# Performance work log

Measured on AMD Instinct MI355X. Metric: run time of the kernel, lower is better.

Reference implementation:

```python
import jax, jax.numpy as jnp
import numpy as np

D_MODEL = 1024
N_HEADS = 16
D_HIDDEN = 4096
EPS = 1e-6
SCALE = float(np.sqrt(D_MODEL // N_HEADS))


def setup_inputs() -> dict:
    key = jax.random.key(0)
    ks = jax.random.split(key, 12)
    d, h = D_MODEL, D_HIDDEN
    init = lambda k, shape, fan_in: jax.random.uniform(k, shape, jnp.float32, -1.0, 1.0) / np.sqrt(fan_in)
    return {
        "x": jax.random.normal(ks[0], (2, 2048, d), jnp.float32),
        "W_q": init(ks[1], (d, d), d),
        "W_k": init(ks[2], (d, d), d),
        "W_v": init(ks[3], (d, d), d),
        "W_o": init(ks[4], (d, d), d),
        "b_o": init(ks[5], (d,), d),
        "attn_norm_w": 1.0 + jax.random.normal(ks[6], (d,), jnp.float32) / np.sqrt(d),
        "ffn_norm_w": 1.0 + jax.random.normal(ks[7], (d,), jnp.float32) / np.sqrt(d),
        "W_gate": init(ks[8], (d, h), d),
        "W_hidden": init(ks[9], (d, h), d),
        "W_out": init(ks[10], (h, d), h),
        "b_out": init(ks[11], (d,), h),
    }


def rmsnorm(x, w):
    return w * x * jax.lax.rsqrt(jnp.mean(x * x, axis=-1, keepdims=True) + EPS)


def attention(x, W_q, W_k, W_v, W_o, b_o):
    b, l, d = x.shape
    hd = d // N_HEADS
    split = lambda t: t.reshape(b, l, N_HEADS, hd).transpose(0, 2, 1, 3)  # b n l d
    q = split(x @ W_q)
    k = split(x @ W_k)
    v = split(x @ W_v)
    scores = jnp.einsum('bnld,bnmd->bnlm', q, k) / SCALE
    attn = jax.nn.softmax(scores, axis=-1)
    out = jnp.einsum('bnlm,bnmd->bnld', attn, v)
    out = out.transpose(0, 2, 1, 3).reshape(b, l, d)
    return out @ W_o + b_o


def swiglu(x, W_gate, W_hidden, W_out, b_out):
    return (jax.nn.silu(x @ W_gate) * (x @ W_hidden)) @ W_out + b_out


def reference(x, W_q, W_k, W_v, W_o, b_o, attn_norm_w, ffn_norm_w, W_gate, W_hidden, W_out, b_out):
    x = x + attention(rmsnorm(x, attn_norm_w), W_q, W_k, W_v, W_o, b_o)
    return x + swiglu(rmsnorm(x, ffn_norm_w), W_gate, W_hidden, W_out, b_out)
```

## Files before the change

kernel.cpp:

```cpp
#include <hip/hip_runtime.h>
#include <stdint.h>
#include <stddef.h>

typedef unsigned short ushort_t;
typedef __attribute__((ext_vector_type(8))) unsigned short us8;
typedef __attribute__((ext_vector_type(4))) unsigned short us4;
typedef __attribute__((ext_vector_type(2))) unsigned int u32x2;
typedef __attribute__((ext_vector_type(8))) short bf16x8;
typedef __attribute__((ext_vector_type(4))) float f32x4;
typedef __attribute__((ext_vector_type(4))) float f4;

#define DM 1024
#define SEQ 2048
#define NBATCH 2
#define NHEADS 16
#define HDIM 64
#define DH 4096
#define ROWS 4096

__device__ __forceinline__ float bf2f(ushort_t u) {
  union { unsigned int i; float f; } v; v.i = ((unsigned int)u) << 16; return v.f;
}
__device__ __forceinline__ ushort_t f2bf(float f) {
  union { float f; unsigned int i; } v; v.f = f;
  unsigned int x = v.i;
  unsigned int r = (x + 0x7FFFu + ((x >> 16) & 1u)) >> 16;
  return (ushort_t)r;
}
__device__ __forceinline__ unsigned int fbits(float f) {
  union { float f; unsigned int i; } v; v.f = f; return v.i;
}

__global__ void transpose_all(const float* __restrict__ Wq, const float* __restrict__ Wk,
                              const float* __restrict__ Wv, const float* __restrict__ Wo,
                              const float* __restrict__ Wg, const float* __restrict__ Wh,
                              const float* __restrict__ Wu,
                              ushort_t* __restrict__ WqkvT, ushort_t* __restrict__ WoT,
                              ushort_t* __restrict__ WghT, ushort_t* __restrict__ WuT) {
  const float* src; ushort_t* dst; int R, C, rowmul = 1, rowoff = 0;
  switch (blockIdx.y) {
    case 0: src = Wq; dst = WqkvT;                R = DM; C = DM; break;
    case 1: src = Wk; dst = WqkvT + DM * DM;      R = DM; C = DM; break;
    case 2: src = Wv; dst = WqkvT + 2 * DM * DM;  R = DM; C = DM; break;
    case 3: src = Wo; dst = WoT;                  R = DM; C = DM; break;
    case 4: src = Wg; dst = WghT;                 R = DM; C = DH; rowmul = 2; rowoff = 0; break;
    case 5: src = Wh; dst = WghT;                 R = DM; C = DH; rowmul = 2; rowoff = 1; break;
    default: src = Wu; dst = WuT;                 R = DH; C = DM; break;
  }
  int nbx = C >> 6, nby = R >> 6;
  int bid = blockIdx.x;
  if (bid >= nbx * nby) return;
  int c0 = (bid % nbx) * 64, r0 = (bid / nbx) * 64;

  __shared__ ushort_t tile[64][68];
  int t = threadIdx.x;
#pragma unroll
  for (int i = 0; i < 4; ++i) {
    int c = i * 256 + t;
    int row = c >> 4, col4 = (c & 15) * 4;
    f4 v = *(const f4*)(src + (size_t)(r0 + row) * C + c0 + col4);
#pragma unroll
    for (int j = 0; j < 4; ++j) tile[row][col4 + j] = f2bf(v[j]);
  }
  __syncthreads();
#pragma unroll
  for (int i = 0; i < 4; ++i) {
    int c = i * 256 + t;
    int orow = c >> 4, col4 = (c & 15) * 4;
    us4 v;
#pragma unroll
    for (int j = 0; j < 4; ++j) v[j] = tile[col4 + j][orow];
    *(us4*)(dst + ((size_t)(c0 + orow) * rowmul + rowoff) * R + r0 + col4) = v;
  }
}

__global__ void rmsnorm_kernel(const float* __restrict__ x,
                               const float* __restrict__ w,
                               ushort_t* __restrict__ y) {
  int row = blockIdx.x;
  int t = threadIdx.x;
  f4 xv = *(const f4*)(x + (size_t)row * DM + t * 4);
  float s = 0.f;
#pragma unroll
  for (int j = 0; j < 4; ++j) s += xv[j] * xv[j];
#pragma unroll
  for (int off = 32; off >= 1; off >>= 1) s += __shfl_xor(s, off);
  __shared__ float wsum[4];
  if ((t & 63) == 0) wsum[t >> 6] = s;
  __syncthreads();
  float tot = wsum[0] + wsum[1] + wsum[2] + wsum[3];
  float scale = rsqrtf(tot * (1.0f / DM) + 1e-6f);
  f4 wv = *(const f4*)(w + t * 4);
  us4 o;
#pragma unroll
  for (int j = 0; j < 4; ++j) o[j] = f2bf(xv[j] * wv[j] * scale);
  *(us4*)(y + (size_t)row * DM + t * 4) = o;
}

template <int EPI, int TM>
__global__ __launch_bounds__(256) void gemm_bt(
    const ushort_t* __restrict__ A, const ushort_t* __restrict__ Bt,
    void* __restrict__ Cv, int M, int N, int K,
    const float* __restrict__ bias, const void* __restrict__ resv) {
  constexpr int FI = TM / 32;
  __shared__ __align__(16) ushort_t As[TM * 64];
  __shared__ __align__(16) ushort_t Bs[128 * 64];
  int tid = threadIdx.x;
  int l = tid & 63, w = tid >> 6;
  int wm = w >> 1, wn = w & 1;
  int m0 = blockIdx.y * TM, n0 = blockIdx.x * 128;
  int lr = l & 15, lk = (l >> 4) * 8;
  f32x4 acc[FI][4] = {};
  const ushort_t* Ag = A + (size_t)m0 * K;
  const ushort_t* Bg = Bt + (size_t)n0 * K;
  int srow = tid >> 3;
  int scol = (tid & 7) * 8;

  for (int kt = 0; kt < K; kt += 64) {
#pragma unroll
    for (int i = 0; i < TM / 32; ++i) {
      __builtin_amdgcn_global_load_lds(
          (const __attribute__((address_space(1))) unsigned int*)(Ag + (size_t)(i * 32 + srow) * K + kt + scol),
          (__attribute__((address_space(3))) unsigned int*)(&As[(i * 256 + tid) * 8]), 16, 0, 0);
    }
#pragma unroll
    for (int i = 0; i < 4; ++i) {
      __builtin_amdgcn_global_load_lds(
          (const __attribute__((address_space(1))) unsigned int*)(Bg + (size_t)(i * 32 + srow) * K + kt + scol),
          (__attribute__((address_space(3))) unsigned int*)(&Bs[(i * 256 + tid) * 8]), 16, 0, 0);
    }
    __syncthreads();
#pragma unroll
    for (int kk = 0; kk < 2; ++kk) {
      bf16x8 a[FI], b[4];
#pragma unroll
      for (int i = 0; i < FI; ++i)
        a[i] = *(const bf16x8*)(&As[(wm * (TM / 2) + i * 16 + lr) * 64 + kk * 32 + lk]);
#pragma unroll
      for (int j = 0; j < 4; ++j)
        b[j] = *(const bf16x8*)(&Bs[(wn * 64 + j * 16 + lr) * 64 + kk * 32 + lk]);
#pragma unroll
      for (int i = 0; i < FI; ++i)
#pragma unroll
        for (int j = 0; j < 4; ++j)
          acc[i][j] = __builtin_amdgcn_mfma_f32_16x16x32_bf16(a[i], b[j], acc[i][j], 0, 0, 0);
    }
    __syncthreads();
  }

  int r0 = (l >> 4) * 4;
#pragma unroll
  for (int i = 0; i < FI; ++i) {
#pragma unroll
    for (int r = 0; r < 4; ++r) {
      int grow = m0 + wm * (TM / 2) + i * 16 + r0 + r;
#pragma unroll
      for (int j = 0; j < 4; ++j) {
        int gcol = n0 + wn * 64 + j * 16 + lr;
        float v = acc[i][j][r];
        if (EPI == 0) {
          ((ushort_t*)Cv)[(size_t)grow * N + gcol] = f2bf(v);
        } else if (EPI == 1) {
          size_t idx = (size_t)grow * N + gcol;
          float r2 = ((const float*)resv)[idx];
          ((float*)Cv)[idx] = v + bias[gcol] + r2;
        } else {
          float o = __shfl_xor(v, 1);
          float gt = (lr & 1) ? o : v;
          float hd = (lr & 1) ? v : o;
          float a = gt / (1.0f + __expf(-gt)) * hd;
          if (!(lr & 1))
            ((ushort_t*)Cv)[(size_t)grow * (N >> 1) + (gcol >> 1)] = f2bf(a);
        }
      }
    }
  }
}

__global__ void vtrans_kernel(const ushort_t* __restrict__ qkv,
                              ushort_t* __restrict__ VT) {
  __shared__ ushort_t tile[64][72];
  int t = threadIdx.x;
  int s0 = blockIdx.x * 64;
  int h = blockIdx.y, b = blockIdx.z;
  const ushort_t* src = qkv + (size_t)b * SEQ * (3 * DM) + 2 * DM + h * HDIM;
  ushort_t* dst = VT + ((size_t)(b * NHEADS + h) * HDIM) * SEQ;
#pragma unroll
  for (int i = 0; i < 2; ++i) {
    int c = i * 256 + t;
    int srow = c >> 3, d8 = (c & 7) * 8;
    *(us8*)(&tile[srow][d8]) = *(const us8*)(src + (size_t)(s0 + srow) * (3 * DM) + d8);
  }
  __syncthreads();
#pragma unroll
  for (int i = 0; i < 2; ++i) {
    int c = i * 256 + t;
    int drow = c >> 3, s8 = (c & 7) * 8;
    us8 v;
#pragma unroll
    for (int j = 0; j < 8; ++j) v[j] = tile[s8 + j][drow];
    *(us8*)(dst + (size_t)drow * SEQ + s0 + s8) = v;
  }
}

#define LDP 72

__global__ __launch_bounds__(256) void attn_mfma(
    const ushort_t* __restrict__ Qp, const ushort_t* __restrict__ Kp,
    const ushort_t* __restrict__ VT, ushort_t* __restrict__ Op,
    int qs, int os) {
  __shared__ __align__(16) ushort_t Qs[64 * LDP];
  __shared__ __align__(16) ushort_t Ks[64 * LDP];
  __shared__ __align__(16) ushort_t Vs[64 * LDP];
  __shared__ __align__(16) ushort_t Ps[4][16 * LDP];
  int tid = threadIdx.x;
  int l = tid & 63;
  int w = tid >> 6;
  int g = l >> 4;
  int q = l & 15;
  int h = blockIdx.y, b = blockIdx.z;
  int q0 = blockIdx.x * 64;
  const size_t base = (size_t)b * SEQ * qs + h * HDIM;
  const size_t obase = (size_t)b * SEQ * os + h * HDIM;
  const ushort_t* Vb = VT + ((size_t)(b * NHEADS + h) * HDIM) * SEQ;

#pragma unroll
  for (int i = 0; i < 2; ++i) {
    int cc = i * 256 + tid;
    int row = cc >> 3, d8 = (cc & 7) * 8;
    *(us8*)(&Qs[row * LDP + d8]) =
        *(const us8*)(Qp + base + (size_t)(q0 + row) * qs + d8);
  }
  __syncthreads();
  bf16x8 qf0 = *(const bf16x8*)(&Qs[(w * 16 + q) * LDP + g * 8]);
  bf16x8 qf1 = *(const bf16x8*)(&Qs[(w * 16 + q) * LDP + 32 + g * 8]);

  const float C1 = 0.125f * 1.44269504f;
  const float C2 = 12.0f * 1.44269504f;
  float l_run = 0.f;
  f32x4 oacc[4] = {};

  for (int kv = 0; kv < SEQ; kv += 64) {
    __syncthreads();
#pragma unroll
    for (int i = 0; i < 2; ++i) {
      int cc = i * 256 + tid;
      int row = cc >> 3, d8 = (cc & 7) * 8;
      *(us8*)(&Ks[row * LDP + d8]) =
          *(const us8*)(Kp + base + (size_t)(kv + row) * qs + d8);
      *(us8*)(&Vs[row * LDP + d8]) =
          *(const us8*)(Vb + (size_t)row * SEQ + kv + d8);
    }
    __syncthreads();

    f32x4 sacc[4] = {};
#pragma unroll
    for (int t = 0; t < 4; ++t) {
      bf16x8 kf0 = *(const bf16x8*)(&Ks[(t * 16 + q) * LDP + g * 8]);
      sacc[t] = __builtin_amdgcn_mfma_f32_16x16x32_bf16(kf0, qf0, sacc[t], 0, 0, 0);
      bf16x8 kf1 = *(const bf16x8*)(&Ks[(t * 16 + q) * LDP + 32 + g * 8]);
      sacc[t] = __builtin_amdgcn_mfma_f32_16x16x32_bf16(kf1, qf1, sacc[t], 0, 0, 0);
    }

    float psum = 0.f;
#pragma unroll
    for (int t = 0; t < 4; ++t) {
      float p0 = exp2f(fmaf(sacc[t][0], C1, -C2));
      float p1 = exp2f(fmaf(sacc[t][1], C1, -C2));
      float p2 = exp2f(fmaf(sacc[t][2], C1, -C2));
      float p3 = exp2f(fmaf(sacc[t][3], C1, -C2));
      psum += (p0 + p1) + (p2 + p3);
      u32x2 d;
      d[0] = __builtin_amdgcn_perm(fbits(p1), fbits(p0), 0x07060302u);
      d[1] = __builtin_amdgcn_perm(fbits(p3), fbits(p2), 0x07060302u);
      *(u32x2*)(&Ps[w][q * LDP + t * 16 + g * 4]) = d;
    }
    l_run += psum;

    __asm__ volatile("s_waitcnt lgkmcnt(0)" ::: "memory");

#pragma unroll
    for (int kk = 0; kk < 2; ++kk) {
      bf16x8 pf = *(const bf16x8*)(&Ps[w][q * LDP + kk * 32 + g * 8]);
#pragma unroll
      for (int t = 0; t < 4; ++t) {
        bf16x8 vf = *(const bf16x8*)(&Vs[(t * 16 + q) * LDP + kk * 32 + g * 8]);
        oacc[t] = __builtin_amdgcn_mfma_f32_16x16x32_bf16(vf, pf, oacc[t], 0, 0, 0);
      }
    }
  }

  l_run += __shfl_xor(l_run, 16);
  l_run += __shfl_xor(l_run, 32);
  float inv = 1.f / l_run;
#pragma unroll
  for (int t = 0; t < 4; ++t) {
    us4 o;
#pragma unroll
    for (int r = 0; r < 4; ++r) o[r] = f2bf(oacc[t][r] * inv);
    *(us4*)(Op + obase + (size_t)(q0 + w * 16 + q) * os + t * 16 + g * 4) = o;
  }
}

extern "C" void kernel_launch(void* const* d_in, const int* in_sizes, int n_in,
                              void* d_out, int out_size, void* d_ws, size_t ws_size,
                              hipStream_t stream) {
  const float* x   = (const float*)d_in[0];
  const float* Wq  = (const float*)d_in[1];
  const float* Wk  = (const float*)d_in[2];
  const float* Wv  = (const float*)d_in[3];
  const float* Wo  = (const float*)d_in[4];
  const float* bo  = (const float*)d_in[5];
  const float* anw = (const float*)d_in[6];
  const float* fnw = (const float*)d_in[7];
  const float* Wg  = (const float*)d_in[8];
  const float* Wh  = (const float*)d_in[9];
  const float* Wu  = (const float*)d_in[10];
  const float* bu  = (const float*)d_in[11];

  char* wsb = (char*)d_ws;
  ushort_t* WqkvT = (ushort_t*)(wsb + 0);
  ushort_t* WoT   = (ushort_t*)(wsb + (6u << 20));
  ushort_t* WghT  = (ushort_t*)(wsb + (8u << 20));
  ushort_t* WuT   = (ushort_t*)(wsb + (24u << 20));
  ushort_t* hb    = (ushort_t*)(wsb + (32u << 20));
  ushort_t* qkvb  = (ushort_t*)(wsb + (40u << 20));
  ushort_t* ab    = (ushort_t*)(wsb + (64u << 20));
  ushort_t* gb    = (ushort_t*)(wsb + (40u << 20));
  ushort_t* VT    = (ushort_t*)d_out;
  float* out = (float*)d_out;

  transpose_all<<<dim3(1024, 7), 256, 0, stream>>>(Wq, Wk, Wv, Wo, Wg, Wh, Wu,
                                                   WqkvT, WoT, WghT, WuT);

  rmsnorm_kernel<<<ROWS, 256, 0, stream>>>(x, anw, hb);
  gemm_bt<0, 128><<<dim3(24, 32), 256, 0, stream>>>(hb, WqkvT, qkvb, ROWS, 3 * DM, DM, nullptr, nullptr);
  vtrans_kernel<<<dim3(SEQ / 64, NHEADS, NBATCH), 256, 0, stream>>>(qkvb, VT);
  attn_mfma<<<dim3(SEQ / 64, NHEADS, NBATCH), 256, 0, stream>>>(
      qkvb, qkvb + DM, VT, ab, 3 * DM, DM);
  gemm_bt<1, 64><<<dim3(8, 64), 256, 0, stream>>>(ab, WoT, out, ROWS, DM, DM, bo, x);

  rmsnorm_kernel<<<ROWS, 256, 0, stream>>>(out, fnw, hb);
  gemm_bt<3, 128><<<dim3(64, 32), 256, 0, stream>>>(hb, WghT, gb, ROWS, 2 * DH, DM, nullptr, nullptr);
  gemm_bt<1, 64><<<dim3(8, 64), 256, 0, stream>>>(gb, WuT, out, ROWS, DM, DH, bu, out);
}
```

Baseline: 486.5 us.

## Load attention K/V fragments straight from global; interleave gate/hidden in 16-row blocks

The attention kernel stops staging Q, K and V tiles in shared memory. Each lane now loads its MFMA fragments directly from global memory, which removes the per-iteration block barriers and LDS round trips. The cost is that all four waves in a block load the same K/V data redundantly and depend on L1/L2 to serve it. Separately, the gate and hidden weights are interleaved in 16-row blocks instead of alternating rows, so the SwiGLU epilogue pairs whole accumulator fragments without cross-lane shuffles and without idle half-lanes on stores.

After: 616.9 us. 1.27x slower.

```diff
diff --git a/kernel.cpp b/kernel.cpp
--- a/kernel.cpp
+++ b/kernel.cpp
@@ -37,14 +37,14 @@
                               const float* __restrict__ Wu,
                               ushort_t* __restrict__ WqkvT, ushort_t* __restrict__ WoT,
                               ushort_t* __restrict__ WghT, ushort_t* __restrict__ WuT) {
-  const float* src; ushort_t* dst; int R, C, rowmul = 1, rowoff = 0;
+  const float* src; ushort_t* dst; int R, C, ilv = 0;
   switch (blockIdx.y) {
     case 0: src = Wq; dst = WqkvT;                R = DM; C = DM; break;
     case 1: src = Wk; dst = WqkvT + DM * DM;      R = DM; C = DM; break;
     case 2: src = Wv; dst = WqkvT + 2 * DM * DM;  R = DM; C = DM; break;
     case 3: src = Wo; dst = WoT;                  R = DM; C = DM; break;
-    case 4: src = Wg; dst = WghT;                 R = DM; C = DH; rowmul = 2; rowoff = 0; break;
-    case 5: src = Wh; dst = WghT;                 R = DM; C = DH; rowmul = 2; rowoff = 1; break;
+    case 4: src = Wg; dst = WghT;                 R = DM; C = DH; ilv = 1; break;
+    case 5: src = Wh; dst = WghT;                 R = DM; C = DH; ilv = 2; break;
     default: src = Wu; dst = WuT;                 R = DH; C = DM; break;
   }
   int nbx = C >> 6, nby = R >> 6;
@@ -70,7 +70,10 @@
     us4 v;
 #pragma unroll
     for (int j = 0; j < 4; ++j) v[j] = tile[col4 + j][orow];
-    *(us4*)(dst + ((size_t)(c0 + orow) * rowmul + rowoff) * R + r0 + col4) = v;
+    int gr = c0 + orow;
+    size_t drow = (ilv == 0) ? (size_t)gr
+                             : (size_t)(gr & ~15) * 2 + (gr & 15) + (ilv == 2 ? 16 : 0);
+    *(us4*)(dst + drow * R + r0 + col4) = v;
   }
 }
 
@@ -154,23 +157,27 @@
 #pragma unroll
     for (int r = 0; r < 4; ++r) {
       int grow = m0 + wm * (TM / 2) + i * 16 + r0 + r;
-#pragma unroll
-      for (int j = 0; j < 4; ++j) {
-        int gcol = n0 + wn * 64 + j * 16 + lr;
-        float v = acc[i][j][r];
-        if (EPI == 0) {
-          ((ushort_t*)Cv)[(size_t)grow * N + gcol] = f2bf(v);
-        } else if (EPI == 1) {
-          size_t idx = (size_t)grow * N + gcol;
-          float r2 = ((const float*)resv)[idx];
-          ((float*)Cv)[idx] = v + bias[gcol] + r2;
-        } else {
-          float o = __shfl_xor(v, 1);
-          float gt = (lr & 1) ? o : v;
-          float hd = (lr & 1) ? v : o;
+      if (EPI == 3) {
+#pragma unroll
+        for (int jp = 0; jp < 2; ++jp) {
+          float gt = acc[i][jp * 2][r];
+          float hd = acc[i][jp * 2 + 1][r];
           float a = gt / (1.0f + __expf(-gt)) * hd;
-          if (!(lr & 1))
-            ((ushort_t*)Cv)[(size_t)grow * (N >> 1) + (gcol >> 1)] = f2bf(a);
+          int acol = (n0 >> 1) + wn * 32 + jp * 16 + lr;
+          ((ushort_t*)Cv)[(size_t)grow * (N >> 1) + acol] = f2bf(a);
+        }
+      } else {
+#pragma unroll
+        for (int j = 0; j < 4; ++j) {
+          int gcol = n0 + wn * 64 + j * 16 + lr;
+          float v = acc[i][j][r];
+          if (EPI == 0) {
+            ((ushort_t*)Cv)[(size_t)grow * N + gcol] = f2bf(v);
+          } else {
+            size_t idx = (size_t)grow * N + gcol;
+            float r2 = ((const float*)resv)[idx];
+            ((float*)Cv)[idx] = v + bias[gcol] + r2;
+          }
         }
       }
     }
@@ -209,31 +216,27 @@
     const ushort_t* __restrict__ Qp, const ushort_t* __restrict__ Kp,
     const ushort_t* __restrict__ VT, ushort_t* __restrict__ Op,
     int qs, int os) {
-  __shared__ __align__(16) ushort_t Qs[64 * LDP];
-  __shared__ __align__(16) ushort_t Ks[64 * LDP];
-  __shared__ __align__(16) ushort_t Vs[64 * LDP];
   __shared__ __align__(16) ushort_t Ps[4][16 * LDP];
   int tid = threadIdx.x;
-  int l = tid & 63;
-  int w = tid >> 6;
-  int g = l >> 4;
-  int q = l & 15;
+  int l = tid & 63, w = tid >> 6;
+  int g = l >> 4, q = l & 15;
   int h = blockIdx.y, b = blockIdx.z;
   int q0 = blockIdx.x * 64;
   const size_t base = (size_t)b * SEQ * qs + h * HDIM;
   const size_t obase = (size_t)b * SEQ * os + h * HDIM;
   const ushort_t* Vb = VT + ((size_t)(b * NHEADS + h) * HDIM) * SEQ;
 
-#pragma unroll
-  for (int i = 0; i < 2; ++i) {
-    int cc = i * 256 + tid;
-    int row = cc >> 3, d8 = (cc & 7) * 8;
-    *(us8*)(&Qs[row * LDP + d8]) =
-        *(const us8*)(Qp + base + (size_t)(q0 + row) * qs + d8);
-  }
-  __syncthreads();
-  bf16x8 qf0 = *(const bf16x8*)(&Qs[(w * 16 + q) * LDP + g * 8]);
-  bf16x8 qf1 = *(const bf16x8*)(&Qs[(w * 16 + q) * LDP + 32 + g * 8]);
+  const ushort_t* Qrow = Qp + base + (size_t)(q0 + w * 16 + q) * qs + g * 8;
+  bf16x8 qf0 = *(const bf16x8*)(Qrow);
+  bf16x8 qf1 = *(const bf16x8*)(Qrow + 32);
+
+  const ushort_t* Kr[4];
+  const ushort_t* Vr[4];
+#pragma unroll
+  for (int t = 0; t < 4; ++t) {
+    Kr[t] = Kp + base + (size_t)(t * 16 + q) * qs + g * 8;
+    Vr[t] = Vb + (size_t)(t * 16 + q) * SEQ + g * 8;
+  }
 
   const float C1 = 0.125f * 1.44269504f;
   const float C2 = 12.0f * 1.44269504f;
@@ -241,25 +244,14 @@
   f32x4 oacc[4] = {};
 
   for (int kv = 0; kv < SEQ; kv += 64) {
-    __syncthreads();
-#pragma unroll
-    for (int i = 0; i < 2; ++i) {
-      int cc = i * 256 + tid;
-      int row = cc >> 3, d8 = (cc & 7) * 8;
-      *(us8*)(&Ks[row * LDP + d8]) =
-          *(const us8*)(Kp + base + (size_t)(kv + row) * qs + d8);
-      *(us8*)(&Vs[row * LDP + d8]) =
-          *(const us8*)(Vb + (size_t)row * SEQ + kv + d8);
-    }
-    __syncthreads();
-
     f32x4 sacc[4] = {};
 #pragma unroll
     for (int t = 0; t < 4; ++t) {
-      bf16x8 kf0 = *(const bf16x8*)(&Ks[(t * 16 + q) * LDP + g * 8]);
+      bf16x8 kf0 = *(const bf16x8*)(Kr[t]);
+      bf16x8 kf1 = *(const bf16x8*)(Kr[t] + 32);
       sacc[t] = __builtin_amdgcn_mfma_f32_16x16x32_bf16(kf0, qf0, sacc[t], 0, 0, 0);
-      bf16x8 kf1 = *(const bf16x8*)(&Ks[(t * 16 + q) * LDP + 32 + g * 8]);
       sacc[t] = __builtin_amdgcn_mfma_f32_16x16x32_bf16(kf1, qf1, sacc[t], 0, 0, 0);
+      Kr[t] += (size_t)64 * qs;
     }
 
     float psum = 0.f;
@@ -284,10 +276,12 @@
       bf16x8 pf = *(const bf16x8*)(&Ps[w][q * LDP + kk * 32 + g * 8]);
 #pragma unroll
       for (int t = 0; t < 4; ++t) {
-        bf16x8 vf = *(const bf16x8*)(&Vs[(t * 16 + q) * LDP + kk * 32 + g * 8]);
+        bf16x8 vf = *(const bf16x8*)(Vr[t] + kk * 32);
         oacc[t] = __builtin_amdgcn_mfma_f32_16x16x32_bf16(vf, pf, oacc[t], 0, 0, 0);
       }
     }
+#pragma unroll
+    for (int t = 0; t < 4; ++t) Vr[t] += 64;
   }
 
   l_run += __shfl_xor(l_run, 16);
```
